# Kernel tuning notes

Hardware: AMD Instinct MI355X
Metric: run time of the kernel (lower is better)

## Reference

```python
import jax, jax.numpy as jnp
import numpy as np

# Bit index 0 = LSB of the IEEE-754 uint32 pattern (little-endian bit order):
# bits[..., 0:23] mantissa, bits[..., 23:31] exponent, bits[..., 31] sign.
_SHIFTS = jnp.arange(32, dtype=jnp.uint32)


def f32_to_bits(x):
    """float32 [...] -> pulse bits [..., 32] in {0., 1.}."""
    u = jax.lax.bitcast_convert_type(x, jnp.uint32)
    return ((u[..., None] >> _SHIFTS) & jnp.uint32(1)).astype(jnp.float32)


def bits_to_f32(b):
    """pulse bits [..., 32] -> float32 [...]. Exact inverse of f32_to_bits."""
    u = jnp.sum(b.astype(jnp.uint32) << _SHIFTS, axis=-1, dtype=jnp.uint32)
    return jax.lax.bitcast_convert_type(u, jnp.float32)


def setup_inputs() -> dict:
    key = jax.random.key(0)
    kA, kB = jax.random.split(key)
    # Encode realistic fp32 values into pulse (bit) tensors.
    A_vals = jax.random.normal(kA, (4, 512, 512), dtype=jnp.float32)   # [B, M, K]
    B_vals = jax.random.normal(kB, (512, 512), dtype=jnp.float32)      # [K, N]
    return {"A": f32_to_bits(A_vals), "B": f32_to_bits(B_vals)}


def reference(A, B):
    """Spike-domain FP32 matmul: decode pulses -> fp32 GEMM -> re-encode pulses.

    A: [..., M, K, 32] pulses, B: [K, N, 32] pulses -> C: [..., M, N, 32] pulses.
    The spiking multiplier/adder gates implement exact IEEE-754 fp32 multiply
    and sequential accumulation over k, i.e. C[..., i, j] = sum_k A[...,i,k]*B[k,j]
    in fp32.
    """
    A_f = bits_to_f32(A)                         # [B, M, K]
    B_f = bits_to_f32(B)                         # [K, N]
    C = jnp.einsum('bmk,kn->bmn', A_f, B_f)      # fp32 accumulation
    return f32_to_bits(C)                        # [B, M, N, 32]
```

## Files before the change

kernel.cpp:

```cpp
#include <hip/hip_runtime.h>
#include <stdint.h>

#define BATCH 4
#define MDIM  512
#define KDIM  512
#define NDIM  512
#define ROWS  (BATCH * MDIM)
#define BR    4
#define BCOLS 256

#define WORDS_A (ROWS * KDIM)
#define WORDS_B (KDIM * NDIM)
#define WORDS_T (WORDS_A + WORDS_B)
#define DEC_BLOCKS 2048
#define DEC_WAVES  (DEC_BLOCKS * 4)
#define DEC_ITERS  (WORDS_T / (32 * DEC_WAVES))

typedef unsigned int u32x4 __attribute__((ext_vector_type(4)));
typedef float        f32x4 __attribute__((ext_vector_type(4)));

__device__ __forceinline__ uint32_t spread4(uint32_t x) {
    x = (x | (x << 12)) & 0x000F000Fu;
    x = (x | (x << 6))  & 0x03030303u;
    x = (x | (x << 3))  & 0x11111111u;
    return x;
}

__global__ __launch_bounds__(256) void decode_all(const float* __restrict__ Abits,
                                                  const float* __restrict__ Bbits,
                                                  uint32_t* __restrict__ Au,
                                                  uint32_t* __restrict__ Bu) {
    const int lane = threadIdx.x & 63;
    const int waveId = (blockIdx.x * blockDim.x + threadIdx.x) >> 6;
    const int sh = lane & 56;

#pragma unroll
    for (int i = 0; i < DEC_ITERS; ++i) {
        const int wb = (waveId + i * DEC_WAVES) * 32;
        const float* src;
        uint32_t* dst;
        if (wb < WORDS_A) { src = Abits + (size_t)wb * 32;             dst = Au + wb; }
        else              { src = Bbits + (size_t)(wb - WORDS_A) * 32; dst = Bu + (wb - WORDS_A); }

        const u32x4* sp = (const u32x4*)src;
        u32x4 v0 = __builtin_nontemporal_load(sp + lane);
        u32x4 v1 = __builtin_nontemporal_load(sp + lane + 64);
        u32x4 v2 = __builtin_nontemporal_load(sp + lane + 128);
        u32x4 v3 = __builtin_nontemporal_load(sp + lane + 192);

        unsigned long long m[16];
        m[0]  = __ballot((v0.x >> 29) & 1u);  m[1]  = __ballot((v0.y >> 29) & 1u);
        m[2]  = __ballot((v0.z >> 29) & 1u);  m[3]  = __ballot((v0.w >> 29) & 1u);
        m[4]  = __ballot((v1.x >> 29) & 1u);  m[5]  = __ballot((v1.y >> 29) & 1u);
        m[6]  = __ballot((v1.z >> 29) & 1u);  m[7]  = __ballot((v1.w >> 29) & 1u);
        m[8]  = __ballot((v2.x >> 29) & 1u);  m[9]  = __ballot((v2.y >> 29) & 1u);
        m[10] = __ballot((v2.z >> 29) & 1u);  m[11] = __ballot((v2.w >> 29) & 1u);
        m[12] = __ballot((v3.x >> 29) & 1u);  m[13] = __ballot((v3.y >> 29) & 1u);
        m[14] = __ballot((v3.z >> 29) & 1u);  m[15] = __ballot((v3.w >> 29) & 1u);

        if ((lane & 7) == 0) {
#pragma unroll
            for (int g = 0; g < 4; ++g) {
                uint32_t w = (spread4((uint32_t)(m[4*g+0] >> sh) & 0xFFu) << 0)
                           | (spread4((uint32_t)(m[4*g+1] >> sh) & 0xFFu) << 1)
                           | (spread4((uint32_t)(m[4*g+2] >> sh) & 0xFFu) << 2)
                           | (spread4((uint32_t)(m[4*g+3] >> sh) & 0xFFu) << 3);
                dst[8 * g + (lane >> 3)] = w;
            }
        }
    }
}

__global__ __launch_bounds__(256) void gemm_encode(const float* __restrict__ A,
                                                   const float* __restrict__ B,
                                                   float* __restrict__ outbits) {
    __shared__ uint32_t Us[BR][BCOLS];

    const int tid = threadIdx.x;
    const int rowBase = blockIdx.x * BR;
    const int n0 = blockIdx.y * BCOLS;
    const int n = n0 + tid;

    float acc[BR];
#pragma unroll
    for (int r = 0; r < BR; ++r) acc[r] = 0.0f;

    const float* Bcol = B + n;
    const float* Arow = A + (size_t)rowBase * KDIM;

    float bn[8], bc[8];
#pragma unroll
    for (int i = 0; i < 8; ++i) bn[i] = Bcol[(size_t)i * NDIM];

#pragma unroll 2
    for (int k0 = 0; k0 < KDIM; k0 += 8) {
#pragma unroll
        for (int i = 0; i < 8; ++i) bc[i] = bn[i];
        const int kp = (k0 + 8) & (KDIM - 1);
#pragma unroll
        for (int i = 0; i < 8; ++i) bn[i] = Bcol[(size_t)(kp + i) * NDIM];

        float4 a0[BR], a1[BR];
#pragma unroll
        for (int r = 0; r < BR; ++r) {
            a0[r] = *(const float4*)(Arow + (size_t)r * KDIM + k0);
            a1[r] = *(const float4*)(Arow + (size_t)r * KDIM + k0 + 4);
        }
#pragma unroll
        for (int r = 0; r < BR; ++r) {
            acc[r] = __builtin_fmaf(a0[r].x, bc[0], acc[r]);
            acc[r] = __builtin_fmaf(a0[r].y, bc[1], acc[r]);
            acc[r] = __builtin_fmaf(a0[r].z, bc[2], acc[r]);
            acc[r] = __builtin_fmaf(a0[r].w, bc[3], acc[r]);
            acc[r] = __builtin_fmaf(a1[r].x, bc[4], acc[r]);
            acc[r] = __builtin_fmaf(a1[r].y, bc[5], acc[r]);
            acc[r] = __builtin_fmaf(a1[r].z, bc[6], acc[r]);
            acc[r] = __builtin_fmaf(a1[r].w, bc[7], acc[r]);
        }
    }

#pragma unroll
    for (int r = 0; r < BR; ++r) Us[r][tid] = __float_as_uint(acc[r]);
    __syncthreads();

    float* oBase = outbits + ((size_t)rowBase * NDIM + n0) * 32;
    const int b = (tid & 7) * 4;
#pragma unroll
    for (int r = 0; r < BR; ++r) {
        float* o = oBase + (size_t)r * NDIM * 32;
#pragma unroll
        for (int it = 0; it < 8; ++it) {
            uint32_t u = Us[r][it * 32 + (tid >> 3)];
            f32x4 q;
            q.x = (float)((u >> (b + 0)) & 1u);
            q.y = (float)((u >> (b + 1)) & 1u);
            q.z = (float)((u >> (b + 2)) & 1u);
            q.w = (float)((u >> (b + 3)) & 1u);
            __builtin_nontemporal_store(q, (f32x4*)(o + it * 1024 + tid * 4));
        }
    }
}

extern "C" void kernel_launch(void* const* d_in, const int* in_sizes, int n_in,
                              void* d_out, int out_size, void* d_ws, size_t ws_size,
                              hipStream_t stream) {
    const float* Abits = (const float*)d_in[0];
    const float* Bbits = (const float*)d_in[1];
    float* out = (float*)d_out;

    uint32_t* A_u = (uint32_t*)d_ws;
    uint32_t* B_u = A_u + WORDS_A;

    decode_all<<<DEC_BLOCKS, 256, 0, stream>>>(Abits, Bbits, A_u, B_u);

    dim3 grid(ROWS / BR, NDIM / BCOLS);
    gemm_encode<<<grid, 256, 0, stream>>>((const float*)A_u, (const float*)B_u, out);
}
```

Baseline: 82.31 us.

## Stage B tiles into LDS with double-buffered direct global-to-LDS loads

The GEMM kernel now copies 16-row chunks of the decoded B matrix into a double-buffered shared-memory tile using async global_load_lds. The next chunk is fetched while the current one is computed, replacing the per-thread register prefetch of B columns from global memory. The aim is to hide B load latency behind compute. In exchange it adds a block barrier per chunk and relies on the barrier correctly waiting for the async LDS writes. The output-encoding scratch space reuses the B buffer.

```diff
diff --git a/kernel.cpp b/kernel.cpp
--- a/kernel.cpp
+++ b/kernel.cpp
@@ -8,6 +8,8 @@
 #define ROWS  (BATCH * MDIM)
 #define BR    4
 #define BCOLS 256
+#define KC    16
+#define NCH   (KDIM / KC)
 
 #define WORDS_A (ROWS * KDIM)
 #define WORDS_B (KDIM * NDIM)
@@ -74,53 +76,70 @@
 __global__ __launch_bounds__(256) void gemm_encode(const float* __restrict__ A,
                                                    const float* __restrict__ B,
                                                    float* __restrict__ outbits) {
-    __shared__ uint32_t Us[BR][BCOLS];
+    __shared__ __align__(16) float Bs[2][KC][BCOLS];
 
     const int tid = threadIdx.x;
     const int rowBase = blockIdx.x * BR;
     const int n0 = blockIdx.y * BCOLS;
-    const int n = n0 + tid;
 
     float acc[BR];
 #pragma unroll
     for (int r = 0; r < BR; ++r) acc[r] = 0.0f;
 
-    const float* Bcol = B + n;
     const float* Arow = A + (size_t)rowBase * KDIM;
 
-    float bn[8], bc[8];
+    auto stage = [&](int buf, int c) {
 #pragma unroll
-    for (int i = 0; i < 8; ++i) bn[i] = Bcol[(size_t)i * NDIM];
+        for (int it = 0; it < (KC * BCOLS) / (256 * 4); ++it) {
+            int ci = it * 1024 + tid * 4;
+            int kk = ci >> 8;
+            int j  = ci & (BCOLS - 1);
+            const float* gsrc = B + (size_t)(c * KC + kk) * NDIM + n0 + j;
+            __builtin_amdgcn_global_load_lds(
+                (const __attribute__((address_space(1))) void*)gsrc,
+                (__attribute__((address_space(3))) void*)(&Bs[buf][0][0] + ci),
+                16, 0, 0);
+        }
+    };
 
-#pragma unroll 2
-    for (int k0 = 0; k0 < KDIM; k0 += 8) {
+    stage(0, 0);
+    __syncthreads();
+
+    for (int c = 0; c < NCH; ++c) {
+        if (c + 1 < NCH) stage((c + 1) & 1, c + 1);
+
+        const int cur = c & 1;
 #pragma unroll
-        for (int i = 0; i < 8; ++i) bc[i] = bn[i];
-        const int kp = (k0 + 8) & (KDIM - 1);
+        for (int g8 = 0; g8 < KC / 8; ++g8) {
+            const int k0 = c * KC + g8 * 8;
+            float bc[8];
 #pragma unroll
-        for (int i = 0; i < 8; ++i) bn[i] = Bcol[(size_t)(kp + i) * NDIM];
+            for (int i = 0; i < 8; ++i) bc[i] = Bs[cur][g8 * 8 + i][tid];
 
-        float4 a0[BR], a1[BR];
+            float4 a0[BR], a1[BR];
 #pragma unroll
-        for (int r = 0; r < BR; ++r) {
-            a0[r] = *(const float4*)(Arow + (size_t)r * KDIM + k0);
-            a1[r] = *(const float4*)(Arow + (size_t)r * KDIM + k0 + 4);
+            for (int r = 0; r < BR; ++r) {
+                a0[r] = *(const float4*)(Arow + (size_t)r * KDIM + k0);
+                a1[r] = *(const float4*)(Arow + (size_t)r * KDIM + k0 + 4);
+            }
+#pragma unroll
+            for (int r = 0; r < BR; ++r) {
+                acc[r] = __builtin_fmaf(a0[r].x, bc[0], acc[r]);
+                acc[r] = __builtin_fmaf(a0[r].y, bc[1], acc[r]);
+                acc[r] = __builtin_fmaf(a0[r].z, bc[2], acc[r]);
+                acc[r] = __builtin_fmaf(a0[r].w, bc[3], acc[r]);
+                acc[r] = __builtin_fmaf(a1[r].x, bc[4], acc[r]);
+                acc[r] = __builtin_fmaf(a1[r].y, bc[5], acc[r]);
+                acc[r] = __builtin_fmaf(a1[r].z, bc[6], acc[r]);
+                acc[r] = __builtin_fmaf(a1[r].w, bc[7], acc[r]);
+            }
         }
-#pragma unroll
-        for (int r = 0; r < BR; ++r) {
-            acc[r] = __builtin_fmaf(a0[r].x, bc[0], acc[r]);
-            acc[r] = __builtin_fmaf(a0[r].y, bc[1], acc[r]);
-            acc[r] = __builtin_fmaf(a0[r].z, bc[2], acc[r]);
-            acc[r] = __builtin_fmaf(a0[r].w, bc[3], acc[r]);
-            acc[r] = __builtin_fmaf(a1[r].x, bc[4], acc[r]);
-            acc[r] = __builtin_fmaf(a1[r].y, bc[5], acc[r]);
-            acc[r] = __builtin_fmaf(a1[r].z, bc[6], acc[r]);
-            acc[r] = __builtin_fmaf(a1[r].w, bc[7], acc[r]);
-        }
+        __syncthreads();
     }
 
+    uint32_t* Us = (uint32_t*)&Bs[0][0][0];
 #pragma unroll
-    for (int r = 0; r < BR; ++r) Us[r][tid] = __float_as_uint(acc[r]);
+    for (int r = 0; r < BR; ++r) Us[r * BCOLS + tid] = __float_as_uint(acc[r]);
     __syncthreads();
 
     float* oBase = outbits + ((size_t)rowBase * NDIM + n0) * 32;
@@ -130,7 +149,7 @@
         float* o = oBase + (size_t)r * NDIM * 32;
 #pragma unroll
         for (int it = 0; it < 8; ++it) {
-            uint32_t u = Us[r][it * 32 + (tid >> 3)];
+            uint32_t u = Us[r * BCOLS + it * 32 + (tid >> 3)];
             f32x4 q;
             q.x = (float)((u >> (b + 0)) & 1u);
             q.y = (float)((u >> (b + 1)) & 1u);
```

Result: faster. 78.53 us, median of 2 (-4.6%).
